# Performance work log

Measured on AMD Instinct MI355X. Metric: run time of the kernel, lower is better.

Reference implementation:

```python
import jax, jax.numpy as jnp
import numpy as np
from jax import lax

NH, KD, AR, RES = 4, 16, 4, 40          # num_heads, key_dim, attn_ratio, resolution
DIM = 256
HD = DIM // NH                           # head_dim = 64
D = AR * KD                              # per-head value dim = 64
N = RES * RES                            # 1600 tokens
B = 16
EPS = 1e-5
SCALE = KD ** -0.5


def _bn(x, g, b, m, v):
    # eval-mode BatchNorm2d over channel dim of [B,C,H,W]
    s = g * lax.rsqrt(v + EPS)
    return (x - m[:, None, None]) * s[:, None, None] + b[:, None, None]


def setup_inputs() -> dict:
    key = jax.random.key(0)
    ks = iter(jax.random.split(key, 40))
    nrm = lambda sh, s=0.05: jax.random.normal(next(ks), sh, jnp.float32) * s
    pos = lambda sh: jax.random.uniform(next(ks), sh, jnp.float32, 0.5, 1.5)
    return {
        "x": jax.random.normal(next(ks), (B, DIM, RES, RES), jnp.float32),
        "dw_w": nrm((NH, HD, 1, 5, 5), 0.1),
        "dw_g": pos((NH, HD)), "dw_b": nrm((NH, HD)), "dw_m": nrm((NH, HD), 0.1), "dw_v": pos((NH, HD)),
        "q_w": nrm((NH, KD, HD), 0.1),
        "q_g": pos((NH, KD)), "q_b": nrm((NH, KD)), "q_m": nrm((NH, KD), 0.1), "q_v": pos((NH, KD)),
        "k_w": nrm((NH, KD, HD), 0.1),
        "k_g": pos((NH, KD)), "k_b": nrm((NH, KD)), "k_m": nrm((NH, KD), 0.1), "k_v": pos((NH, KD)),
        "v_w": nrm((NH, D, HD), 0.1),
        "v_g": pos((NH, D)), "v_b": nrm((NH, D)), "v_m": nrm((NH, D), 0.1), "v_v": pos((NH, D)),
        "proj_w": nrm((DIM, D * NH), 0.05),
        "proj_g": pos((DIM,)), "proj_b": nrm((DIM,)), "proj_m": nrm((DIM,), 0.1), "proj_v": pos((DIM,)),
        "attn_bias": nrm((NH, N), 0.02),
    }


def reference(x, dw_w, dw_g, dw_b, dw_m, dw_v,
              q_w, q_g, q_b, q_m, q_v,
              k_w, k_g, k_b, k_m, k_v,
              v_w, v_g, v_b, v_m, v_v,
              proj_w, proj_g, proj_b, proj_m, proj_v,
              attn_bias):
    Bx, C, H, W = x.shape
    Nx = H * W
    x_heads = jnp.split(x, NH, axis=1)   # NH x [B, HD, H, W]
    outs, prev = [], None
    for i in range(NH):
        # depthwise 5x5 conv + BN
        xi = lax.conv_general_dilated(
            x_heads[i], dw_w[i], window_strides=(1, 1), padding='SAME',
            feature_group_count=HD, dimension_numbers=('NCHW', 'OIHW', 'NCHW'))
        xi = _bn(xi, dw_g[i], dw_b[i], dw_m[i], dw_v[i])
        if prev is not None:
            xi = xi + prev                       # cascading residual
        # 1x1 conv projections + BN
        q = _bn(jnp.einsum('kc,bchw->bkhw', q_w[i], xi), q_g[i], q_b[i], q_m[i], q_v[i])
        k = _bn(jnp.einsum('kc,bchw->bkhw', k_w[i], xi), k_g[i], k_b[i], k_m[i], k_v[i])
        v = _bn(jnp.einsum('dc,bchw->bdhw', v_w[i], xi), v_g[i], v_b[i], v_m[i], v_v[i])
        qf = q.reshape(Bx, KD, Nx).transpose(0, 2, 1)   # [B, N, KD]
        kf = k.reshape(Bx, KD, Nx)                      # [B, KD, N]
        vf = v.reshape(Bx, D, Nx).transpose(0, 2, 1)    # [B, N, D]
        attn = jnp.einsum('bnk,bkm->bnm', qf, kf) * SCALE
        attn = attn + attn_bias[i][None, None, :]
        attn = jax.nn.softmax(attn, axis=-1)
        out = jnp.einsum('bnm,bmd->bnd', attn, vf).transpose(0, 2, 1).reshape(Bx, D, H, W)
        outs.append(out)
        prev = out[:, :HD]
    o = jnp.concatenate(outs, axis=1)                  # [B, D*NH, H, W]
    o = _bn(jnp.einsum('oc,bchw->bohw', proj_w, o), proj_g, proj_b, proj_m, proj_v)
    return jax.nn.relu(o)
```

## Files before the change

kernel.cpp:

```cpp
#include <hip/hip_runtime.h>
#include <cstddef>

namespace {
constexpr int kNH  = 4;
constexpr int kKD  = 16;
constexpr int kHD  = 64;
constexpr int kD   = 64;
constexpr int kRES = 40;
constexpr int kN   = 1600;
constexpr int kB   = 16;
constexpr int kDIM = 256;
constexpr int kQT  = kN / 32;
constexpr float kEPS   = 1e-5f;
constexpr float kSCALE = 0.25f;
constexpr float kLOG2E = 1.4426950408889634f;
constexpr float kC1    = kSCALE * kLOG2E;
}

typedef __attribute__((ext_vector_type(8)))  short short8;
typedef __attribute__((ext_vector_type(4)))  short s16x4;
typedef __attribute__((ext_vector_type(4)))  float f32x4;
typedef __attribute__((ext_vector_type(16))) float f32x16;

static __device__ __forceinline__ unsigned short f2bf(float x) {
  unsigned u = __builtin_bit_cast(unsigned, x);
  u = (u + 0x7fffu + ((u >> 16) & 1u)) >> 16;
  return (unsigned short)u;
}
static __device__ __forceinline__ float bf2f(unsigned short b) {
  return __builtin_bit_cast(float, (unsigned)b << 16);
}

struct Params {
  const float *x, *dw_w, *dw_g, *dw_b, *dw_m, *dw_v;
  const float *q_w, *q_g, *q_b, *q_m, *q_v;
  const float *k_w, *k_g, *k_b, *k_m, *k_v;
  const float *v_w, *v_g, *v_b, *v_m, *v_v;
  const float *proj_w, *proj_g, *proj_b, *proj_m, *proj_v, *attn_bias;
  float *bias2, *psc, *psh, *qkv_sc, *qkv_sh;
  unsigned short *q_t, *k_t, *v_p, *o_bf, *w_bf, *x_t, *w_qk, *w_vv;
  float *out;
};

static __device__ __forceinline__ void prep_body(int i, const Params& p) {
  if (i < kNH * kN) p.bias2[i] = p.attn_bias[i] * kLOG2E;
  if (i < kDIM * kDIM) p.w_bf[i] = f2bf(p.proj_w[i]);
  if (i < kDIM) {
    const float sc = p.proj_g[i] * rsqrtf(p.proj_v[i] + kEPS);
    p.psc[i] = sc;
    p.psh[i] = p.proj_b[i] - p.proj_m[i] * sc;
  }
  if (i < kNH * 32 * kHD) {
    const int head = i >> 11;
    const int ch = (i >> 6) & 31;
    const int c = i & 63;
    const float wv = (ch < 16) ? p.q_w[head * 1024 + ch * 64 + c]
                               : p.k_w[head * 1024 + (ch - 16) * 64 + c];
    p.w_qk[i] = f2bf(wv);
  }
  if (i < kNH * kD * kHD) p.w_vv[i] = f2bf(p.v_w[i]);
  if (i < kNH * 96) {
    const int head = i / 96;
    const int ch = i - head * 96;
    float g, bb, mm, vv;
    if (ch < 16) {
      const int r = head * 16 + ch;
      g = p.q_g[r]; bb = p.q_b[r]; mm = p.q_m[r]; vv = p.q_v[r];
    } else if (ch < 32) {
      const int r = head * 16 + (ch - 16);
      g = p.k_g[r]; bb = p.k_b[r]; mm = p.k_m[r]; vv = p.k_v[r];
    } else {
      const int r = head * 64 + (ch - 32);
      g = p.v_g[r]; bb = p.v_b[r]; mm = p.v_m[r]; vv = p.v_v[r];
    }
    const float sc = g * rsqrtf(vv + kEPS);
    p.qkv_sc[i] = sc;
    p.qkv_sh[i] = bb - mm * sc;
  }
}

__global__ __launch_bounds__(256) void conv_prep_kernel(Params p) {
  const int blk = blockIdx.x;
  const int tid = threadIdx.x;
  if (blk < 256) prep_body(blk * 256 + tid, p);

  __shared__ float P[44 * 44];
  const int b = blk >> 8;
  const int gc = blk & 255;
  const int head = gc >> 6;
  const int c = gc & 63;

  for (int i = tid; i < 44 * 44; i += 256) P[i] = 0.f;
  __syncthreads();

  const float* xin = p.x + ((size_t)b * kDIM + gc) * kN;
  for (int i = tid; i < kN; i += 256) {
    const int r = i / kRES;
    const int col = i - r * kRES;
    P[(r + 2) * 44 + col + 2] = xin[i];
  }

  float wreg[25];
  const float* wc = p.dw_w + (size_t)gc * 25;
#pragma unroll
  for (int t = 0; t < 25; ++t) wreg[t] = wc[t];
  const float sc = p.dw_g[gc] * rsqrtf(p.dw_v[gc] + kEPS);
  const float sh = p.dw_b[gc] - p.dw_m[gc] * sc;

  __syncthreads();

  if (tid < 200) {
    const int h = tid / 5;
    const int w0 = (tid - h * 5) * 8;
    float acc[8] = {};
#pragma unroll
    for (int dh = 0; dh < 5; ++dh) {
      float t[12];
      const float* row = P + (h + dh) * 44 + w0;
#pragma unroll
      for (int i = 0; i < 12; ++i) t[i] = row[i];
#pragma unroll
      for (int j = 0; j < 8; ++j)
#pragma unroll
        for (int i = 0; i < 5; ++i)
          acc[j] = fmaf(t[j + i], wreg[dh * 5 + i], acc[j]);
    }
    unsigned short* xr = p.x_t + (size_t)head * kB * kN * 64 +
                         (((size_t)b * kN) + h * kRES + w0) * 64 + c;
#pragma unroll
    for (int j = 0; j < 8; ++j)
      xr[(size_t)j * 64] = f2bf(acc[j] * sc + sh);
  }
}

__global__ __launch_bounds__(256) void qkv_all_kernel(Params p) {
  const int lane = threadIdx.x & 63;
  const int head = blockIdx.x / 600;
  const int w = (blockIdx.x - head * 600) * 4 + (threadIdx.x >> 6);
  const unsigned short* x_t = p.x_t + (size_t)head * kB * kN * 64;
  const unsigned short* w_qk = p.w_qk + (size_t)head * 32 * kHD;
  const unsigned short* w_v = p.w_vv + (size_t)head * kD * kHD;
  const float* qsc = p.qkv_sc + head * 96;
  const float* qsh = p.qkv_sh + head * 96;
  unsigned short* q_t = p.q_t + (size_t)head * kB * kN * kKD;
  unsigned short* k_t = p.k_t + (size_t)head * kB * kN * kKD;
  unsigned short* v_p = p.v_p + (size_t)head * kB * kD * kN;

  const int b = w / 150;
  const int r = w - b * 150;
  const int col = lane & 31;
  const int h = lane >> 5;

  if (r < kQT) {
    const int n0 = r * 32;
    const unsigned short* ax = w_qk + (size_t)col * 64 + h * 8;
    const unsigned short* bx = x_t + ((size_t)b * kN + n0 + col) * 64 + h * 8;
    f32x16 acc = {};
#pragma unroll
    for (int kk = 0; kk < 4; ++kk) {
      const short8 af = *(const short8*)(ax + kk * 16);
      const short8 bf = *(const short8*)(bx + kk * 16);
      acc = __builtin_amdgcn_mfma_f32_32x32x16_bf16(af, bf, acc, 0, 0, 0);
    }
    const int n = n0 + col;
    unsigned short* qrow = q_t + ((size_t)b * kN + n) * 16;
    unsigned short* krow = k_t + ((size_t)b * kN + n) * 16;
#pragma unroll
    for (int g = 0; g < 4; ++g) {
      const int ch0 = g * 8 + 4 * h;
      const f32x4 s4 = *(const f32x4*)(qsc + ch0);
      const f32x4 h4 = *(const f32x4*)(qsh + ch0);
      s16x4 pk;
#pragma unroll
      for (int j = 0; j < 4; ++j)
        pk[j] = (short)f2bf(acc[g * 4 + j] * s4[j] + h4[j]);
      if (ch0 < 16) *(s16x4*)(qrow + ch0) = pk;
      else          *(s16x4*)(krow + ch0 - 16) = pk;
    }
  } else {
    const int idx = r - kQT;
    const int dt = idx / kQT;
    const int nt = idx - dt * kQT;
    const int n0 = nt * 32;
    const int d = dt * 32 + col;
    const unsigned short* ax = x_t + ((size_t)b * kN + n0 + col) * 64 + h * 8;
    const unsigned short* bx = w_v + (size_t)d * 64 + h * 8;
    f32x16 acc = {};
#pragma unroll
    for (int kk = 0; kk < 4; ++kk) {
      const short8 af = *(const short8*)(ax + kk * 16);
      const short8 bf = *(const short8*)(bx + kk * 16);
      acc = __builtin_amdgcn_mfma_f32_32x32x16_bf16(af, bf, acc, 0, 0, 0);
    }
    const float sc = qsc[32 + d];
    const float sh = qsh[32 + d];
    unsigned short* vrow = v_p + ((size_t)(b * kD) + d) * kN + n0;
#pragma unroll
    for (int g = 0; g < 4; ++g) {
      const int rr0 = g * 8 + 4 * h;
      const int low = rr0 & 15;
      const int pos = (rr0 & 16) | (low & 3) | ((low & 4) << 1) |
                      ((low & 8) >> 1);
      s16x4 pk;
#pragma unroll
      for (int j = 0; j < 4; ++j)
        pk[j] = (short)f2bf(acc[g * 4 + j] * sc + sh);
      *(s16x4*)(vrow + pos) = pk;
    }
  }
}

__global__ __launch_bounds__(256) void attn_fused_kernel(Params p, int head) {
  __shared__ float so[4][64][33];
  __shared__ float sml[4][32][2];
  __shared__ unsigned short o_lds[32][72];
  const int tid = threadIdx.x;
  const int lane = tid & 63;
  const int wv = tid >> 6;
  const int blk = blockIdx.x;
  const int b = blk / kQT;
  const int qt = blk - b * kQT;
  const int col = lane & 31;
  const int h = lane >> 5;
  const int nq = qt * 32 + col;

  const unsigned short* q_t = p.q_t + (size_t)head * kB * kN * kKD;
  const unsigned short* k_t = p.k_t + (size_t)head * kB * kN * kKD;
  const unsigned short* v_p = p.v_p + (size_t)head * kB * kD * kN;

  const short8 qf =
      *(const short8*)(q_t + ((size_t)b * kN + nq) * 16 + h * 8);
  const float* bs = p.bias2 + (size_t)head * kN;
  const unsigned short* vb0 = v_p + ((size_t)(b * kD) + col) * kN;
  const unsigned short* vb1 = v_p + ((size_t)(b * kD) + 32 + col) * kN;

  f32x16 o0 = {}, o1 = {};
  float m = -3.0e38f, l = 0.f;

  for (int kt = wv; kt < kQT; kt += 4) {
    const int kb = kt * 32;
    const short8 kf =
        *(const short8*)(k_t + ((size_t)b * kN + kb + col) * 16 + h * 8);
    f32x16 c = {};
    c = __builtin_amdgcn_mfma_f32_32x32x16_bf16(kf, qf, c, 0, 0, 0);

    const f32x4 bv0 = *(const f32x4*)(bs + kb + 4 * h);
    const f32x4 bv1 = *(const f32x4*)(bs + kb + 8 + 4 * h);
    const f32x4 bv2 = *(const f32x4*)(bs + kb + 16 + 4 * h);
    const f32x4 bv3 = *(const f32x4*)(bs + kb + 24 + 4 * h);

    float s[16];
#pragma unroll
    for (int r = 0; r < 4; ++r)  s[r]      = fmaf(c[r],      kC1, bv0[r]);
#pragma unroll
    for (int r = 0; r < 4; ++r)  s[4 + r]  = fmaf(c[4 + r],  kC1, bv1[r]);
#pragma unroll
    for (int r = 0; r < 4; ++r)  s[8 + r]  = fmaf(c[8 + r],  kC1, bv2[r]);
#pragma unroll
    for (int r = 0; r < 4; ++r)  s[12 + r] = fmaf(c[12 + r], kC1, bv3[r]);

    float tmax = s[0];
#pragma unroll
    for (int r = 1; r < 16; ++r) tmax = fmaxf(tmax, s[r]);
    tmax = fmaxf(tmax, __shfl_xor(tmax, 32));

    const bool upd = tmax > m + 8.0f;
    if (__any(upd)) {
      const float alpha = upd ? exp2f(m - tmax) : 1.0f;
      m = upd ? tmax : m;
      l *= alpha;
#pragma unroll
      for (int r = 0; r < 16; ++r) { o0[r] *= alpha; o1[r] *= alpha; }
    }

    short8 p0, p1;
    float lsum = 0.f;
#pragma unroll
    for (int e = 0; e < 8; ++e) {
      const float pe = exp2f(s[e] - m);
      lsum += pe;
      p0[e] = (short)f2bf(pe);
    }
#pragma unroll
    for (int e = 0; e < 8; ++e) {
      const float pe = exp2f(s[8 + e] - m);
      lsum += pe;
      p1[e] = (short)f2bf(pe);
    }
    l += lsum;

    const short8 vf00 = *(const short8*)(vb0 + kb + h * 8);
    const short8 vf01 = *(const short8*)(vb0 + kb + 16 + h * 8);
    const short8 vf10 = *(const short8*)(vb1 + kb + h * 8);
    const short8 vf11 = *(const short8*)(vb1 + kb + 16 + h * 8);
    o0 = __builtin_amdgcn_mfma_f32_32x32x16_bf16(vf00, p0, o0, 0, 0, 0);
    o0 = __builtin_amdgcn_mfma_f32_32x32x16_bf16(vf01, p1, o0, 0, 0, 0);
    o1 = __builtin_amdgcn_mfma_f32_32x32x16_bf16(vf10, p0, o1, 0, 0, 0);
    o1 = __builtin_amdgcn_mfma_f32_32x32x16_bf16(vf11, p1, o1, 0, 0, 0);
  }

  l += __shfl_xor(l, 32);

#pragma unroll
  for (int r = 0; r < 16; ++r) {
    so[wv][lane][r] = o0[r];
    so[wv][lane][16 + r] = o1[r];
  }
  if (h == 0) {
    sml[wv][col][0] = m;
    sml[wv][col][1] = l;
  }
  __syncthreads();

  float mc[4], lc[4];
  float M = -3.0e38f;
#pragma unroll
  for (int c = 0; c < 4; ++c) {
    mc[c] = sml[c][col][0];
    lc[c] = sml[c][col][1];
    M = fmaxf(M, mc[c]);
  }
  float scale[4];
  float lt = 0.f;
#pragma unroll
  for (int c = 0; c < 4; ++c) {
    scale[c] = exp2f(mc[c] - M);
    lt = fmaf(lc[c], scale[c], lt);
  }
  const float inv = 1.0f / lt;

  const int r0 = wv * 8;
  float ov[8];
#pragma unroll
  for (int j = 0; j < 8; ++j) {
    float a = 0.f;
#pragma unroll
    for (int c = 0; c < 4; ++c) a = fmaf(so[c][lane][r0 + j], scale[c], a);
    ov[j] = a * inv;
  }

  const int d0a = wv * 16 + 4 * h;
  const int d0b = d0a + 8;
#pragma unroll
  for (int j = 0; j < 4; ++j) {
    o_lds[col][d0a + j] = f2bf(ov[j]);
    o_lds[col][d0b + j] = f2bf(ov[4 + j]);
  }
  if (head < 3) {
    unsigned short* obf = p.o_bf + ((size_t)b * kN + nq) * kDIM + head * kD;
    s16x4 pa, pb;
#pragma unroll
    for (int j = 0; j < 4; ++j) {
      pa[j] = (short)f2bf(ov[j]);
      pb[j] = (short)f2bf(ov[4 + j]);
    }
    *(s16x4*)(obf + d0a) = pa;
    *(s16x4*)(obf + d0b) = pb;
  }
  __syncthreads();

  if (head < 3) {
    const float* scn = p.qkv_sc + (head + 1) * 96;
    if (wv == 0) {
      const unsigned short* aw = p.w_qk + (size_t)(head + 1) * 32 * kHD +
                                 (size_t)col * 64 + h * 8;
      f32x16 acc = {};
#pragma unroll
      for (int kk = 0; kk < 4; ++kk) {
        const short8 af = *(const short8*)(aw + kk * 16);
        const short8 bf = *(const short8*)(&o_lds[col][kk * 16 + h * 8]);
        acc = __builtin_amdgcn_mfma_f32_32x32x16_bf16(af, bf, acc, 0, 0, 0);
      }
      unsigned short* qrow = p.q_t + (size_t)(head + 1) * kB * kN * kKD +
                             ((size_t)b * kN + nq) * 16;
      unsigned short* krow = p.k_t + (size_t)(head + 1) * kB * kN * kKD +
                             ((size_t)b * kN + nq) * 16;
#pragma unroll
      for (int r = 0; r < 16; ++r) {
        const int ch = (r & 3) + 8 * (r >> 2) + 4 * h;
        unsigned short* tp = (ch < 16) ? (qrow + ch) : (krow + ch - 16);
        *tp = f2bf(bf2f(*tp) + acc[r] * scn[ch]);
      }
    } else if (wv <= 2) {
      const int dbase = (wv - 1) * 32;
      const unsigned short* aw = p.w_vv + (size_t)(head + 1) * kD * kHD +
                                 (size_t)(dbase + col) * 64 + h * 8;
      f32x16 acc = {};
#pragma unroll
      for (int kk = 0; kk < 4; ++kk) {
        const short8 af = *(const short8*)(aw + kk * 16);
        const short8 bf = *(const short8*)(&o_lds[col][kk * 16 + h * 8]);
        acc = __builtin_amdgcn_mfma_f32_32x32x16_bf16(af, bf, acc, 0, 0, 0);
      }
      const int ml_ = nq & 15;
      const int pos =
          (nq & ~15) | (ml_ & 3) | ((ml_ & 4) << 1) | ((ml_ & 8) >> 1);
      unsigned short* vbase = p.v_p + (size_t)(head + 1) * kB * kD * kN;
#pragma unroll
      for (int r = 0; r < 16; ++r) {
        const int d = dbase + (r & 3) + 8 * (r >> 2) + 4 * h;
        unsigned short* tp = vbase + ((size_t)(b * kD) + d) * kN + pos;
        *tp = f2bf(bf2f(*tp) + acc[r] * scn[32 + d]);
      }
    }
  } else {
    const unsigned short* brow = p.o_bf + ((size_t)b * kN + nq) * kDIM;
#pragma unroll
    for (int gi = 0; gi < 2; ++gi) {
      const int g = wv * 2 + gi;
      const unsigned short* arow =
          p.w_bf + (size_t)(g * 32 + col) * kDIM + h * 8;
      f32x16 acc = {};
#pragma unroll
      for (int kk = 0; kk < 12; ++kk) {
        const short8 af = *(const short8*)(arow + kk * 16);
        const short8 bf = *(const short8*)(brow + kk * 16 + h * 8);
        acc = __builtin_amdgcn_mfma_f32_32x32x16_bf16(af, bf, acc, 0, 0, 0);
      }
#pragma unroll
      for (int kk = 12; kk < 16; ++kk) {
        const short8 af = *(const short8*)(arow + kk * 16);
        const short8 bf =
            *(const short8*)(&o_lds[col][(kk - 12) * 16 + h * 8]);
        acc = __builtin_amdgcn_mfma_f32_32x32x16_bf16(af, bf, acc, 0, 0, 0);
      }
#pragma unroll
      for (int r = 0; r < 16; ++r) {
        const int o = g * 32 + (r & 3) + 8 * (r >> 2) + 4 * h;
        const float v = acc[r] * p.psc[o] + p.psh[o];
        p.out[((size_t)b * kDIM + o) * kN + nq] = fmaxf(v, 0.f);
      }
    }
  }
}

extern "C" void kernel_launch(void* const* d_in, const int* in_sizes, int n_in,
                              void* d_out, int out_size, void* d_ws,
                              size_t ws_size, hipStream_t stream) {
  Params p;
  p.x      = (const float*)d_in[0];
  p.dw_w   = (const float*)d_in[1];
  p.dw_g   = (const float*)d_in[2];
  p.dw_b   = (const float*)d_in[3];
  p.dw_m   = (const float*)d_in[4];
  p.dw_v   = (const float*)d_in[5];
  p.q_w    = (const float*)d_in[6];
  p.q_g    = (const float*)d_in[7];
  p.q_b    = (const float*)d_in[8];
  p.q_m    = (const float*)d_in[9];
  p.q_v    = (const float*)d_in[10];
  p.k_w    = (const float*)d_in[11];
  p.k_g    = (const float*)d_in[12];
  p.k_b    = (const float*)d_in[13];
  p.k_m    = (const float*)d_in[14];
  p.k_v    = (const float*)d_in[15];
  p.v_w    = (const float*)d_in[16];
  p.v_g    = (const float*)d_in[17];
  p.v_b    = (const float*)d_in[18];
  p.v_m    = (const float*)d_in[19];
  p.v_v    = (const float*)d_in[20];
  p.proj_w = (const float*)d_in[21];
  p.proj_g = (const float*)d_in[22];
  p.proj_b = (const float*)d_in[23];
  p.proj_m = (const float*)d_in[24];
  p.proj_v = (const float*)d_in[25];
  p.attn_bias = (const float*)d_in[26];

  float* ws = (float*)d_ws;
  p.bias2  = ws;
  p.psc    = p.bias2 + kNH * kN;
  p.psh    = p.psc + kDIM;
  p.qkv_sc = p.psh + kDIM;
  p.qkv_sh = p.qkv_sc + kNH * 96;
  p.q_t  = (unsigned short*)(p.qkv_sh + kNH * 96);
  p.k_t  = p.q_t + (size_t)kNH * kB * kN * kKD;
  p.v_p  = p.k_t + (size_t)kNH * kB * kN * kKD;
  p.o_bf = p.v_p + (size_t)kNH * kB * kD * kN;
  p.w_bf = p.o_bf + (size_t)kB * kN * kDIM;
  p.x_t  = p.w_bf + (size_t)kDIM * kDIM;
  p.w_qk = p.x_t + (size_t)kNH * kB * kN * 64;
  p.w_vv = p.w_qk + (size_t)kNH * 32 * kHD;
  p.out = (float*)d_out;

  conv_prep_kernel<<<kB * kDIM, 256, 0, stream>>>(p);
  qkv_all_kernel<<<kNH * 600, 256, 0, stream>>>(p);
  for (int head = 0; head < kNH; ++head)
    attn_fused_kernel<<<kB * kQT, 256, 0, stream>>>(p, head);
}
```

Measured before the change: 367.0 us.

## Compute next-head QKV in attention epilogue from conv plus residual, drop per-head precompute

```diff
diff --git a/kernel.cpp b/kernel.cpp
--- a/kernel.cpp
+++ b/kernel.cpp
@@ -133,18 +133,14 @@
   }
 }
 
-__global__ __launch_bounds__(256) void qkv_all_kernel(Params p) {
+__global__ __launch_bounds__(256) void qkv0_kernel(Params p) {
   const int lane = threadIdx.x & 63;
-  const int head = blockIdx.x / 600;
-  const int w = (blockIdx.x - head * 600) * 4 + (threadIdx.x >> 6);
-  const unsigned short* x_t = p.x_t + (size_t)head * kB * kN * 64;
-  const unsigned short* w_qk = p.w_qk + (size_t)head * 32 * kHD;
-  const unsigned short* w_v = p.w_vv + (size_t)head * kD * kHD;
-  const float* qsc = p.qkv_sc + head * 96;
-  const float* qsh = p.qkv_sh + head * 96;
-  unsigned short* q_t = p.q_t + (size_t)head * kB * kN * kKD;
-  unsigned short* k_t = p.k_t + (size_t)head * kB * kN * kKD;
-  unsigned short* v_p = p.v_p + (size_t)head * kB * kD * kN;
+  const int w = blockIdx.x * 4 + (threadIdx.x >> 6);
+  const unsigned short* x_t = p.x_t;
+  const unsigned short* w_qk = p.w_qk;
+  const unsigned short* w_v = p.w_vv;
+  const float* qsc = p.qkv_sc;
+  const float* qsh = p.qkv_sh;
 
   const int b = w / 150;
   const int r = w - b * 150;
@@ -163,8 +159,8 @@
       acc = __builtin_amdgcn_mfma_f32_32x32x16_bf16(af, bf, acc, 0, 0, 0);
     }
     const int n = n0 + col;
-    unsigned short* qrow = q_t + ((size_t)b * kN + n) * 16;
-    unsigned short* krow = k_t + ((size_t)b * kN + n) * 16;
+    unsigned short* qrow = p.q_t + ((size_t)b * kN + n) * 16;
+    unsigned short* krow = p.k_t + ((size_t)b * kN + n) * 16;
 #pragma unroll
     for (int g = 0; g < 4; ++g) {
       const int ch0 = g * 8 + 4 * h;
@@ -194,7 +190,7 @@
     }
     const float sc = qsc[32 + d];
     const float sh = qsh[32 + d];
-    unsigned short* vrow = v_p + ((size_t)(b * kD) + d) * kN + n0;
+    unsigned short* vrow = p.v_p + ((size_t)(b * kD) + d) * kN + n0;
 #pragma unroll
     for (int g = 0; g < 4; ++g) {
       const int rr0 = g * 8 + 4 * h;
@@ -213,7 +209,7 @@
 __global__ __launch_bounds__(256) void attn_fused_kernel(Params p, int head) {
   __shared__ float so[4][64][33];
   __shared__ float sml[4][32][2];
-  __shared__ unsigned short o_lds[32][72];
+  __shared__ unsigned short xo_lds[32][72];
   const int tid = threadIdx.x;
   const int lane = tid & 63;
   const int wv = tid >> 6;
@@ -341,34 +337,43 @@
 
   const int d0a = wv * 16 + 4 * h;
   const int d0b = d0a + 8;
-#pragma unroll
-  for (int j = 0; j < 4; ++j) {
-    o_lds[col][d0a + j] = f2bf(ov[j]);
-    o_lds[col][d0b + j] = f2bf(ov[4 + j]);
-  }
+
   if (head < 3) {
     unsigned short* obf = p.o_bf + ((size_t)b * kN + nq) * kDIM + head * kD;
+    const unsigned short* xc = p.x_t + (size_t)(head + 1) * kB * kN * 64 +
+                               ((size_t)b * kN + nq) * 64;
+    const s16x4 ca = *(const s16x4*)(xc + d0a);
+    const s16x4 cb4 = *(const s16x4*)(xc + d0b);
     s16x4 pa, pb;
 #pragma unroll
     for (int j = 0; j < 4; ++j) {
       pa[j] = (short)f2bf(ov[j]);
       pb[j] = (short)f2bf(ov[4 + j]);
+      xo_lds[col][d0a + j] = f2bf(bf2f((unsigned short)ca[j]) + ov[j]);
+      xo_lds[col][d0b + j] = f2bf(bf2f((unsigned short)cb4[j]) + ov[4 + j]);
     }
     *(s16x4*)(obf + d0a) = pa;
     *(s16x4*)(obf + d0b) = pb;
+  } else {
+#pragma unroll
+    for (int j = 0; j < 4; ++j) {
+      xo_lds[col][d0a + j] = f2bf(ov[j]);
+      xo_lds[col][d0b + j] = f2bf(ov[4 + j]);
+    }
   }
   __syncthreads();
 
   if (head < 3) {
     const float* scn = p.qkv_sc + (head + 1) * 96;
+    const float* shn = p.qkv_sh + (head + 1) * 96;
     if (wv == 0) {
-      const unsigned short* aw = p.w_qk + (size_t)(head + 1) * 32 * kHD +
+      const unsigned short* ax = p.w_qk + (size_t)(head + 1) * 32 * kHD +
                                  (size_t)col * 64 + h * 8;
       f32x16 acc = {};
 #pragma unroll
       for (int kk = 0; kk < 4; ++kk) {
-        const short8 af = *(const short8*)(aw + kk * 16);
-        const short8 bf = *(const short8*)(&o_lds[col][kk * 16 + h * 8]);
+        const short8 af = *(const short8*)(ax + kk * 16);
+        const short8 bf = *(const short8*)(&xo_lds[col][kk * 16 + h * 8]);
         acc = __builtin_amdgcn_mfma_f32_32x32x16_bf16(af, bf, acc, 0, 0, 0);
       }
       unsigned short* qrow = p.q_t + (size_t)(head + 1) * kB * kN * kKD +
@@ -376,31 +381,44 @@
       unsigned short* krow = p.k_t + (size_t)(head + 1) * kB * kN * kKD +
                              ((size_t)b * kN + nq) * 16;
 #pragma unroll
-      for (int r = 0; r < 16; ++r) {
-        const int ch = (r & 3) + 8 * (r >> 2) + 4 * h;
-        unsigned short* tp = (ch < 16) ? (qrow + ch) : (krow + ch - 16);
-        *tp = f2bf(bf2f(*tp) + acc[r] * scn[ch]);
+      for (int g = 0; g < 4; ++g) {
+        const int ch0 = g * 8 + 4 * h;
+        const f32x4 s4 = *(const f32x4*)(scn + ch0);
+        const f32x4 h4 = *(const f32x4*)(shn + ch0);
+        s16x4 pk;
+#pragma unroll
+        for (int j = 0; j < 4; ++j)
+          pk[j] = (short)f2bf(acc[g * 4 + j] * s4[j] + h4[j]);
+        if (ch0 < 16) *(s16x4*)(qrow + ch0) = pk;
+        else          *(s16x4*)(krow + ch0 - 16) = pk;
       }
     } else if (wv <= 2) {
-      const int dbase = (wv - 1) * 32;
-      const unsigned short* aw = p.w_vv + (size_t)(head + 1) * kD * kHD +
-                                 (size_t)(dbase + col) * 64 + h * 8;
+      const int dt = wv - 1;
+      const int d = dt * 32 + col;
+      const unsigned short* bx = p.w_vv + (size_t)(head + 1) * kD * kHD +
+                                 (size_t)d * 64 + h * 8;
       f32x16 acc = {};
 #pragma unroll
       for (int kk = 0; kk < 4; ++kk) {
-        const short8 af = *(const short8*)(aw + kk * 16);
-        const short8 bf = *(const short8*)(&o_lds[col][kk * 16 + h * 8]);
+        const short8 af = *(const short8*)(&xo_lds[col][kk * 16 + h * 8]);
+        const short8 bf = *(const short8*)(bx + kk * 16);
         acc = __builtin_amdgcn_mfma_f32_32x32x16_bf16(af, bf, acc, 0, 0, 0);
       }
-      const int ml_ = nq & 15;
-      const int pos =
-          (nq & ~15) | (ml_ & 3) | ((ml_ & 4) << 1) | ((ml_ & 8) >> 1);
-      unsigned short* vbase = p.v_p + (size_t)(head + 1) * kB * kD * kN;
-#pragma unroll
-      for (int r = 0; r < 16; ++r) {
-        const int d = dbase + (r & 3) + 8 * (r >> 2) + 4 * h;
-        unsigned short* tp = vbase + ((size_t)(b * kD) + d) * kN + pos;
-        *tp = f2bf(bf2f(*tp) + acc[r] * scn[32 + d]);
+      const float sc = scn[32 + d];
+      const float sh = shn[32 + d];
+      unsigned short* vrow = p.v_p + (size_t)(head + 1) * kB * kD * kN +
+                             ((size_t)(b * kD) + d) * kN + qt * 32;
+#pragma unroll
+      for (int g = 0; g < 4; ++g) {
+        const int rr0 = g * 8 + 4 * h;
+        const int low = rr0 & 15;
+        const int pos = (rr0 & 16) | (low & 3) | ((low & 4) << 1) |
+                        ((low & 8) >> 1);
+        s16x4 pk;
+#pragma unroll
+        for (int j = 0; j < 4; ++j)
+          pk[j] = (short)f2bf(acc[g * 4 + j] * sc + sh);
+        *(s16x4*)(vrow + pos) = pk;
       }
     }
   } else {
@@ -421,7 +439,7 @@
       for (int kk = 12; kk < 16; ++kk) {
         const short8 af = *(const short8*)(arow + kk * 16);
         const short8 bf =
-            *(const short8*)(&o_lds[col][(kk - 12) * 16 + h * 8]);
+            *(const short8*)(&xo_lds[col][(kk - 12) * 16 + h * 8]);
         acc = __builtin_amdgcn_mfma_f32_32x32x16_bf16(af, bf, acc, 0, 0, 0);
       }
 #pragma unroll
@@ -483,7 +501,7 @@
   p.out = (float*)d_out;
 
   conv_prep_kernel<<<kB * kDIM, 256, 0, stream>>>(p);
-  qkv_all_kernel<<<kNH * 600, 256, 0, stream>>>(p);
+  qkv0_kernel<<<600, 256, 0, stream>>>(p);
   for (int head = 0; head < kNH; ++head)
     attn_fused_kernel<<<kB * kQT, 256, 0, stream>>>(p, head);
 }
```

Result: no change. 364.4 us (-0.7%).
